# Optimization experiments

Hardware: AMD Instinct MI355X
Metric: run time of the kernel (lower is better)

The kernel has to match this reference:

```python
import jax, jax.numpy as jnp
import numpy as np


def setup_inputs() -> dict:
    key = jax.random.key(0)
    k1, k2 = jax.random.split(key)
    STATE_LEN, SEQ_LEN, HIDDEN = 8192, 8192, 1024
    out_state = jax.random.normal(k1, (STATE_LEN, HIDDEN), dtype=jnp.float32)
    history = jax.random.normal(k2, (SEQ_LEN, HIDDEN), dtype=jnp.float32)
    return {"out_state": out_state, "history": history}


def reference(out_state, history):
    # attn_energies[i, j] = dot(out_state[i], history[j])  ->  single GEMM
    energies = jnp.einsum('ih,jh->ij', out_state, history)  # [state_len, seq_len]
    # legacy F.softmax on a 2D tensor normalizes along dim=1 (the seq_len axis)
    return jax.nn.softmax(energies, axis=-1)
```

## Files before the change

kernel.cpp:

```cpp
#include <hip/hip_runtime.h>
#include <hip/hip_bf16.h>

#define M 8192
#define N 8192
#define K 1024
#define BM 128
#define BN 128
#define BK 64

typedef __attribute__((ext_vector_type(8))) short short8;
typedef __attribute__((ext_vector_type(4))) float f32x4;

__device__ inline short f2bf(float x){
    __hip_bfloat16 h = __float2bfloat16(x);
    short s; __builtin_memcpy(&s, &h, 2); return s;
}
__device__ inline float bf2f(short s){
    __hip_bfloat16 h; __builtin_memcpy(&h, &s, 2);
    return __bfloat162float(h);
}

__device__ inline void conv8(float4 x0, float4 x1, short8& hi, short8& lo){
    float xs[8] = {x0.x,x0.y,x0.z,x0.w,x1.x,x1.y,x1.z,x1.w};
    #pragma unroll
    for (int j=0;j<8;++j){
        short h = f2bf(xs[j]);
        float r = xs[j] - bf2f(h);
        hi[j] = h; lo[j] = f2bf(r);
    }
}

__global__ __launch_bounds__(256) void presplit(
    const float* __restrict__ A, const float* __restrict__ B,
    short* __restrict__ Ah, short* __restrict__ Al,
    short* __restrict__ Bh, short* __restrict__ Bl)
{
    size_t c = (size_t)blockIdx.x * 256 + threadIdx.x;
    const float* src; short *dh, *dl; size_t off;
    const size_t perMat = (size_t)M * K / 8;
    if (c < perMat){ src = A; dh = Ah; dl = Al; off = c * 8; }
    else           { src = B; dh = Bh; dl = Bl; off = (c - perMat) * 8; }
    float4 x0 = *(const float4*)(src + off);
    float4 x1 = *(const float4*)(src + off + 4);
    short8 hi, lo;
    conv8(x0, x1, hi, lo);
    *(short8*)(dh + off) = hi;
    *(short8*)(dl + off) = lo;
}

#define GLOAD_LDS16(gp, lp) \
    __builtin_amdgcn_global_load_lds((const __attribute__((address_space(1))) void*)(gp), \
                                     (__attribute__((address_space(3))) void*)(lp), 16, 0, 0)

template<int MODE>
__global__ __launch_bounds__(256, 2)
void gemm_kernel(const float* __restrict__ A, const float* __restrict__ B,
                 const short* __restrict__ Ahg, const short* __restrict__ Alg,
                 const short* __restrict__ Bhg, const short* __restrict__ Blg,
                 float* __restrict__ C)
{
    __shared__ __align__(16) short sAh[BM*BK];
    __shared__ __align__(16) short sAl[BM*BK];
    __shared__ __align__(16) short sBh[BM*BK];
    __shared__ __align__(16) short sBl[BM*BK];

    const int tid  = threadIdx.x;
    const int lane = tid & 63, wid = tid >> 6;
    const int bm0 = blockIdx.y * BM, bn0 = blockIdx.x * BN;
    const int wr = wid >> 1, wc = wid & 1;
    const int fr = lane & 15, fg = lane >> 4;

    f32x4 acc[4][4] = {};

    for (int kt = 0; kt < K/BK; ++kt){
        if constexpr (MODE == 0){
            #pragma unroll
            for (int i = 0; i < 4; ++i){
                int bs = wid * 256 + i * 64;
                int s  = bs + lane;
                int row = s >> 3, sp = s & 7;
                int col8 = sp ^ (row & 7);
                size_t ga = (size_t)(bm0 + row) * K + kt * BK + col8 * 8;
                size_t gb = (size_t)(bn0 + row) * K + kt * BK + col8 * 8;
                GLOAD_LDS16(Ahg + ga, &sAh[bs * 8]);
                GLOAD_LDS16(Alg + ga, &sAl[bs * 8]);
                GLOAD_LDS16(Bhg + gb, &sBh[bs * 8]);
                GLOAD_LDS16(Blg + gb, &sBl[bs * 8]);
            }
        } else {
            #pragma unroll
            for (int i = 0; i < 4; ++i){
                int s = tid + i * 256;
                int row = s >> 3, sp = s & 7;
                int widx = row * BK + ((sp ^ (row & 7)) << 3);
                const float* ga = A + (size_t)(bm0 + row) * K + kt * BK + sp * 8;
                float4 a0 = *(const float4*)ga, a1 = *(const float4*)(ga + 4);
                short8 hi, lo;
                conv8(a0, a1, hi, lo);
                *(short8*)&sAh[widx] = hi;
                *(short8*)&sAl[widx] = lo;
                const float* gb = B + (size_t)(bn0 + row) * K + kt * BK + sp * 8;
                float4 b0 = *(const float4*)gb, b1 = *(const float4*)(gb + 4);
                conv8(b0, b1, hi, lo);
                *(short8*)&sBh[widx] = hi;
                *(short8*)&sBl[widx] = lo;
            }
        }
        __syncthreads();

        #pragma unroll
        for (int ks = 0; ks < 2; ++ks){
            short8 ah[4], al[4], bh[4], bl[4];
            #pragma unroll
            for (int m = 0; m < 4; ++m){
                int row = wr * 64 + m * 16 + fr;
                int idx = row * BK + ((((ks << 2) | fg) ^ (row & 7)) << 3);
                ah[m] = *(const short8*)&sAh[idx];
                al[m] = *(const short8*)&sAl[idx];
            }
            #pragma unroll
            for (int n = 0; n < 4; ++n){
                int row = wc * 64 + n * 16 + fr;
                int idx = row * BK + ((((ks << 2) | fg) ^ (row & 7)) << 3);
                bh[n] = *(const short8*)&sBh[idx];
                bl[n] = *(const short8*)&sBl[idx];
            }
            #pragma unroll
            for (int m = 0; m < 4; ++m){
                #pragma unroll
                for (int n = 0; n < 4; ++n){
                    acc[m][n] = __builtin_amdgcn_mfma_f32_16x16x32_bf16(ah[m], bh[n], acc[m][n], 0, 0, 0);
                    acc[m][n] = __builtin_amdgcn_mfma_f32_16x16x32_bf16(ah[m], bl[n], acc[m][n], 0, 0, 0);
                    acc[m][n] = __builtin_amdgcn_mfma_f32_16x16x32_bf16(al[m], bh[n], acc[m][n], 0, 0, 0);
                }
            }
        }
        __syncthreads();
    }

    #pragma unroll
    for (int m = 0; m < 4; ++m){
        int grow_base = bm0 + wr * 64 + m * 16 + fg * 4;
        #pragma unroll
        for (int r = 0; r < 4; ++r){
            float* crow = C + (size_t)(grow_base + r) * N + bn0 + wc * 64 + fr;
            #pragma unroll
            for (int n = 0; n < 4; ++n)
                crow[n * 16] = acc[m][n][r];
        }
    }
}

__global__ __launch_bounds__(256) void row_stats(const float* __restrict__ E, float* __restrict__ stats)
{
    const int row = blockIdx.x;
    const int tid = threadIdx.x;
    const int lane = tid & 63, wid = tid >> 6;
    const float4* rp = (const float4*)(E + (size_t)row * N);
    float4 v[8];
    float mx = -3.4e38f;
    #pragma unroll
    for (int i = 0; i < 8; ++i){
        v[i] = rp[tid + i * 256];
        mx = fmaxf(mx, fmaxf(fmaxf(v[i].x, v[i].y), fmaxf(v[i].z, v[i].w)));
    }
    #pragma unroll
    for (int off = 32; off; off >>= 1) mx = fmaxf(mx, __shfl_xor(mx, off));
    __shared__ float redm[4], reds[4];
    if (lane == 0) redm[wid] = mx;
    __syncthreads();
    mx = fmaxf(fmaxf(redm[0], redm[1]), fmaxf(redm[2], redm[3]));
    float s = 0.f;
    #pragma unroll
    for (int i = 0; i < 8; ++i)
        s += __expf(v[i].x - mx) + __expf(v[i].y - mx) + __expf(v[i].z - mx) + __expf(v[i].w - mx);
    #pragma unroll
    for (int off = 32; off; off >>= 1) s += __shfl_xor(s, off);
    if (lane == 0) reds[wid] = s;
    __syncthreads();
    if (tid == 0){
        stats[2 * row]     = mx;
        stats[2 * row + 1] = reds[0] + reds[1] + reds[2] + reds[3];
    }
}

__global__ __launch_bounds__(256) void normalize(float* __restrict__ E, const float* __restrict__ stats)
{
    size_t idx = (size_t)blockIdx.x * 256 + threadIdx.x;
    int row = (int)(idx >> 11);
    float m = stats[2 * row];
    float inv = 1.0f / stats[2 * row + 1];
    float4 v = ((const float4*)E)[idx];
    v.x = __expf(v.x - m) * inv;
    v.y = __expf(v.y - m) * inv;
    v.z = __expf(v.z - m) * inv;
    v.w = __expf(v.w - m) * inv;
    ((float4*)E)[idx] = v;
}

extern "C" void kernel_launch(void* const* d_in, const int* in_sizes, int n_in,
                              void* d_out, int out_size, void* d_ws, size_t ws_size,
                              hipStream_t stream)
{
    const float* A = (const float*)d_in[0];
    const float* B = (const float*)d_in[1];
    float* out = (float*)d_out;

    const size_t elems = (size_t)M * K;
    const size_t splitBytes = 4 * elems * sizeof(short);
    const size_t statsBytes = (size_t)M * 2 * sizeof(float);

    if (ws_size >= splitBytes + statsBytes){
        short* Ah = (short*)d_ws;
        short* Al = Ah + elems;
        short* Bh = Al + elems;
        short* Bl = Bh + elems;
        float* stats = (float*)(Bl + elems);
        presplit<<<8192, 256, 0, stream>>>(A, B, Ah, Al, Bh, Bl);
        gemm_kernel<0><<<dim3(N/BN, M/BM), 256, 0, stream>>>(A, B, Ah, Al, Bh, Bl, out);
        row_stats<<<M, 256, 0, stream>>>(out, stats);
        normalize<<<(size_t)M * N / 4 / 256, 256, 0, stream>>>(out, stats);
    } else {
        float* stats = (float*)d_ws;
        gemm_kernel<1><<<dim3(N/BN, M/BM), 256, 0, stream>>>(A, B, nullptr, nullptr, nullptr, nullptr, out);
        row_stats<<<M, 256, 0, stream>>>(out, stats);
        normalize<<<(size_t)M * N / 4 / 256, 256, 0, stream>>>(out, stats);
    }
}
```

Measured before the change: 481.8 us.

## Double-buffer GEMM with 8 waves, XCD-aware tile swizzle, and fused single-pass softmax

Replaces the presplit-path GEMM with a 512-thread kernel that double-buffers LDS tiles, so the next K-slice is fetched with global_load_lds while MFMAs run on the current one. It also remaps block indices so tiles sharing rows and columns land on the same XCD for L2 reuse, and raises MFMA priority with s_setprio. The separate row_stats and normalize kernels are merged into one softmax kernel that keeps exponentials in registers and writes normalized values once, removing a full extra read and write of the 256MB output. Double buffering doubles LDS use to 128KB per block, which may limit occupancy.

Measured after the change: 466.3 us. 1.03x faster.

```diff
diff --git a/kernel.cpp b/kernel.cpp
--- a/kernel.cpp
+++ b/kernel.cpp
@@ -7,6 +7,7 @@
 #define BM 128
 #define BN 128
 #define BK 64
+#define ARR (BM*BK)
 
 typedef __attribute__((ext_vector_type(8))) short short8;
 typedef __attribute__((ext_vector_type(4))) float f32x4;
@@ -52,17 +53,110 @@
     __builtin_amdgcn_global_load_lds((const __attribute__((address_space(1))) void*)(gp), \
                                      (__attribute__((address_space(3))) void*)(lp), 16, 0, 0)
 
-template<int MODE>
+__global__ __launch_bounds__(512, 2)
+void gemm_db(const short* __restrict__ Ahg, const short* __restrict__ Alg,
+             const short* __restrict__ Bhg, const short* __restrict__ Blg,
+             float* __restrict__ C)
+{
+    __shared__ __align__(16) short lds[2][4][ARR];
+
+    const int tid  = threadIdx.x;
+    const int lane = tid & 63, wid = tid >> 6;
+
+    const int hw  = blockIdx.x;
+    const int xcd = hw & 7;
+    const int ix  = hw >> 3;
+    const int gst = xcd * 32 + (ix >> 4);
+    const int pos = ix & 15;
+    const int bm0 = ((gst >> 4) * 4 + (pos >> 2)) * BM;
+    const int bn0 = ((gst & 15) * 4 + (pos & 3)) * BN;
+
+    const int wr = wid >> 2, wc = wid & 3;
+    const int fr = lane & 15, fg = lane >> 4;
+
+    f32x4 acc[4][2] = {};
+
+    auto STAGE = [&](int buf, int kt){
+        #pragma unroll
+        for (int i = 0; i < 2; ++i){
+            int bs = wid * 128 + i * 64;
+            int s  = bs + lane;
+            int row = s >> 3, sp = s & 7;
+            int col8 = sp ^ (row & 7);
+            size_t ga = (size_t)(bm0 + row) * K + kt * BK + col8 * 8;
+            size_t gb = (size_t)(bn0 + row) * K + kt * BK + col8 * 8;
+            GLOAD_LDS16(Ahg + ga, &lds[buf][0][bs * 8]);
+            GLOAD_LDS16(Alg + ga, &lds[buf][1][bs * 8]);
+            GLOAD_LDS16(Bhg + gb, &lds[buf][2][bs * 8]);
+            GLOAD_LDS16(Blg + gb, &lds[buf][3][bs * 8]);
+        }
+    };
+
+    STAGE(0, 0);
+    __syncthreads();
+    int cur = 0;
+
+    for (int kt = 0; kt < K/BK; ++kt){
+        if (kt + 1 < K/BK) STAGE(cur ^ 1, kt + 1);
+
+        const short* sAh = lds[cur][0];
+        const short* sAl = lds[cur][1];
+        const short* sBh = lds[cur][2];
+        const short* sBl = lds[cur][3];
+
+        #pragma unroll
+        for (int ks = 0; ks < 2; ++ks){
+            short8 ah[4], al[4], bh[2], bl[2];
+            #pragma unroll
+            for (int m = 0; m < 4; ++m){
+                int row = wr * 64 + m * 16 + fr;
+                int idx = row * BK + ((((ks << 2) | fg) ^ (row & 7)) << 3);
+                ah[m] = *(const short8*)&sAh[idx];
+                al[m] = *(const short8*)&sAl[idx];
+            }
+            #pragma unroll
+            for (int n = 0; n < 2; ++n){
+                int row = wc * 32 + n * 16 + fr;
+                int idx = row * BK + ((((ks << 2) | fg) ^ (row & 7)) << 3);
+                bh[n] = *(const short8*)&sBh[idx];
+                bl[n] = *(const short8*)&sBl[idx];
+            }
+            __builtin_amdgcn_s_setprio(1);
+            #pragma unroll
+            for (int m = 0; m < 4; ++m){
+                #pragma unroll
+                for (int n = 0; n < 2; ++n){
+                    acc[m][n] = __builtin_amdgcn_mfma_f32_16x16x32_bf16(ah[m], bh[n], acc[m][n], 0, 0, 0);
+                    acc[m][n] = __builtin_amdgcn_mfma_f32_16x16x32_bf16(ah[m], bl[n], acc[m][n], 0, 0, 0);
+                    acc[m][n] = __builtin_amdgcn_mfma_f32_16x16x32_bf16(al[m], bh[n], acc[m][n], 0, 0, 0);
+                }
+            }
+            __builtin_amdgcn_s_setprio(0);
+        }
+        __syncthreads();
+        cur ^= 1;
+    }
+
+    #pragma unroll
+    for (int m = 0; m < 4; ++m){
+        int grow = bm0 + wr * 64 + m * 16 + fg * 4;
+        #pragma unroll
+        for (int r = 0; r < 4; ++r){
+            float* crow = C + (size_t)(grow + r) * N + bn0 + wc * 32 + fr;
+            crow[0]  = acc[m][0][r];
+            crow[16] = acc[m][1][r];
+        }
+    }
+}
+
 __global__ __launch_bounds__(256, 2)
-void gemm_kernel(const float* __restrict__ A, const float* __restrict__ B,
-                 const short* __restrict__ Ahg, const short* __restrict__ Alg,
-                 const short* __restrict__ Bhg, const short* __restrict__ Blg,
-                 float* __restrict__ C)
-{
-    __shared__ __align__(16) short sAh[BM*BK];
-    __shared__ __align__(16) short sAl[BM*BK];
-    __shared__ __align__(16) short sBh[BM*BK];
-    __shared__ __align__(16) short sBl[BM*BK];
+void gemm_fb(const float* __restrict__ A, const float* __restrict__ B,
+             float* __restrict__ C)
+{
+    __shared__ __align__(16) short sAh[ARR];
+    __shared__ __align__(16) short sAl[ARR];
+    __shared__ __align__(16) short sBh[ARR];
+    __shared__ __align__(16) short sBl[ARR];
 
     const int tid  = threadIdx.x;
     const int lane = tid & 63, wid = tid >> 6;
@@ -73,38 +167,22 @@
     f32x4 acc[4][4] = {};
 
     for (int kt = 0; kt < K/BK; ++kt){
-        if constexpr (MODE == 0){
-            #pragma unroll
-            for (int i = 0; i < 4; ++i){
-                int bs = wid * 256 + i * 64;
-                int s  = bs + lane;
-                int row = s >> 3, sp = s & 7;
-                int col8 = sp ^ (row & 7);
-                size_t ga = (size_t)(bm0 + row) * K + kt * BK + col8 * 8;
-                size_t gb = (size_t)(bn0 + row) * K + kt * BK + col8 * 8;
-                GLOAD_LDS16(Ahg + ga, &sAh[bs * 8]);
-                GLOAD_LDS16(Alg + ga, &sAl[bs * 8]);
-                GLOAD_LDS16(Bhg + gb, &sBh[bs * 8]);
-                GLOAD_LDS16(Blg + gb, &sBl[bs * 8]);
-            }
-        } else {
-            #pragma unroll
-            for (int i = 0; i < 4; ++i){
-                int s = tid + i * 256;
-                int row = s >> 3, sp = s & 7;
-                int widx = row * BK + ((sp ^ (row & 7)) << 3);
-                const float* ga = A + (size_t)(bm0 + row) * K + kt * BK + sp * 8;
-                float4 a0 = *(const float4*)ga, a1 = *(const float4*)(ga + 4);
-                short8 hi, lo;
-                conv8(a0, a1, hi, lo);
-                *(short8*)&sAh[widx] = hi;
-                *(short8*)&sAl[widx] = lo;
-                const float* gb = B + (size_t)(bn0 + row) * K + kt * BK + sp * 8;
-                float4 b0 = *(const float4*)gb, b1 = *(const float4*)(gb + 4);
-                conv8(b0, b1, hi, lo);
-                *(short8*)&sBh[widx] = hi;
-                *(short8*)&sBl[widx] = lo;
-            }
+        #pragma unroll
+        for (int i = 0; i < 4; ++i){
+            int s = tid + i * 256;
+            int row = s >> 3, sp = s & 7;
+            int widx = row * BK + ((sp ^ (row & 7)) << 3);
+            const float* ga = A + (size_t)(bm0 + row) * K + kt * BK + sp * 8;
+            float4 a0 = *(const float4*)ga, a1 = *(const float4*)(ga + 4);
+            short8 hi, lo;
+            conv8(a0, a1, hi, lo);
+            *(short8*)&sAh[widx] = hi;
+            *(short8*)&sAl[widx] = lo;
+            const float* gb = B + (size_t)(bn0 + row) * K + kt * BK + sp * 8;
+            float4 b0 = *(const float4*)gb, b1 = *(const float4*)(gb + 4);
+            conv8(b0, b1, hi, lo);
+            *(short8*)&sBh[widx] = hi;
+            *(short8*)&sBl[widx] = lo;
         }
         __syncthreads();
 
@@ -140,10 +218,10 @@
 
     #pragma unroll
     for (int m = 0; m < 4; ++m){
-        int grow_base = bm0 + wr * 64 + m * 16 + fg * 4;
+        int grow = bm0 + wr * 64 + m * 16 + fg * 4;
         #pragma unroll
         for (int r = 0; r < 4; ++r){
-            float* crow = C + (size_t)(grow_base + r) * N + bn0 + wc * 64 + fr;
+            float* crow = C + (size_t)(grow + r) * N + bn0 + wc * 64 + fr;
             #pragma unroll
             for (int n = 0; n < 4; ++n)
                 crow[n * 16] = acc[m][n][r];
@@ -151,12 +229,12 @@
     }
 }
 
-__global__ __launch_bounds__(256) void row_stats(const float* __restrict__ E, float* __restrict__ stats)
+__global__ __launch_bounds__(256) void softmax_fused(float* __restrict__ E)
 {
     const int row = blockIdx.x;
     const int tid = threadIdx.x;
     const int lane = tid & 63, wid = tid >> 6;
-    const float4* rp = (const float4*)(E + (size_t)row * N);
+    float4* rp = (float4*)(E + (size_t)row * N);
     float4 v[8];
     float mx = -3.4e38f;
     #pragma unroll
@@ -172,30 +250,22 @@
     mx = fmaxf(fmaxf(redm[0], redm[1]), fmaxf(redm[2], redm[3]));
     float s = 0.f;
     #pragma unroll
-    for (int i = 0; i < 8; ++i)
-        s += __expf(v[i].x - mx) + __expf(v[i].y - mx) + __expf(v[i].z - mx) + __expf(v[i].w - mx);
+    for (int i = 0; i < 8; ++i){
+        v[i].x = __expf(v[i].x - mx); v[i].y = __expf(v[i].y - mx);
+        v[i].z = __expf(v[i].z - mx); v[i].w = __expf(v[i].w - mx);
+        s += v[i].x + v[i].y + v[i].z + v[i].w;
+    }
     #pragma unroll
     for (int off = 32; off; off >>= 1) s += __shfl_xor(s, off);
     if (lane == 0) reds[wid] = s;
     __syncthreads();
-    if (tid == 0){
-        stats[2 * row]     = mx;
-        stats[2 * row + 1] = reds[0] + reds[1] + reds[2] + reds[3];
-    }
-}
-
-__global__ __launch_bounds__(256) void normalize(float* __restrict__ E, const float* __restrict__ stats)
-{
-    size_t idx = (size_t)blockIdx.x * 256 + threadIdx.x;
-    int row = (int)(idx >> 11);
-    float m = stats[2 * row];
-    float inv = 1.0f / stats[2 * row + 1];
-    float4 v = ((const float4*)E)[idx];
-    v.x = __expf(v.x - m) * inv;
-    v.y = __expf(v.y - m) * inv;
-    v.z = __expf(v.z - m) * inv;
-    v.w = __expf(v.w - m) * inv;
-    ((float4*)E)[idx] = v;
+    float inv = 1.0f / (reds[0] + reds[1] + reds[2] + reds[3]);
+    #pragma unroll
+    for (int i = 0; i < 8; ++i){
+        float4 o = v[i];
+        o.x *= inv; o.y *= inv; o.z *= inv; o.w *= inv;
+        rp[tid + i * 256] = o;
+    }
 }
 
 extern "C" void kernel_launch(void* const* d_in, const int* in_sizes, int n_in,
@@ -208,22 +278,16 @@
 
     const size_t elems = (size_t)M * K;
     const size_t splitBytes = 4 * elems * sizeof(short);
-    const size_t statsBytes = (size_t)M * 2 * sizeof(float);
-
-    if (ws_size >= splitBytes + statsBytes){
+
+    if (ws_size >= splitBytes){
         short* Ah = (short*)d_ws;
         short* Al = Ah + elems;
         short* Bh = Al + elems;
         short* Bl = Bh + elems;
-        float* stats = (float*)(Bl + elems);
         presplit<<<8192, 256, 0, stream>>>(A, B, Ah, Al, Bh, Bl);
-        gemm_kernel<0><<<dim3(N/BN, M/BM), 256, 0, stream>>>(A, B, Ah, Al, Bh, Bl, out);
-        row_stats<<<M, 256, 0, stream>>>(out, stats);
-        normalize<<<(size_t)M * N / 4 / 256, 256, 0, stream>>>(out, stats);
+        gemm_db<<<(M/BM)*(N/BN), 512, 0, stream>>>(Ah, Al, Bh, Bl, out);
     } else {
-        float* stats = (float*)d_ws;
-        gemm_kernel<1><<<dim3(N/BN, M/BM), 256, 0, stream>>>(A, B, nullptr, nullptr, nullptr, nullptr, out);
-        row_stats<<<M, 256, 0, stream>>>(out, stats);
-        normalize<<<(size_t)M * N / 4 / 256, 256, 0, stream>>>(out, stats);
-    }
-}
+        gemm_fb<<<dim3(N/BN, M/BM), 256, 0, stream>>>(A, B, out);
+    }
+    softmax_fused<<<M, 256, 0, stream>>>(out);
+}
```
